# Performance work log

Measured on AMD Instinct MI355X. Metric: run time of the kernel, lower is better.

## Reference

```python
import jax, jax.numpy as jnp
import numpy as np

N, DEG, F_IN, H = 50000, 16, 128, 32
E = N * DEG


def _linear_params(key, out_f, in_f):
    kw, kb = jax.random.split(key)
    s = 1.0 / np.sqrt(in_f)
    W = jax.random.uniform(kw, (out_f, in_f), jnp.float32, -s, s)
    b = jax.random.uniform(kb, (out_f,), jnp.float32, -s, s)
    return W, b


def setup_inputs() -> dict:
    key = jax.random.key(0)
    ks = jax.random.split(key, 12)
    X = jax.random.normal(ks[0], (N, F_IN), jnp.float32)
    # DEG distinct nonzero offsets shared by all rows -> unique (src,dst) pairs,
    # so the COO tensor is already coalesced (no duplicate indices).
    offsets = jax.random.permutation(ks[1], jnp.arange(1, N))[:DEG]
    src = jnp.repeat(jnp.arange(N, dtype=jnp.int32), DEG)
    dst = ((src.reshape(N, DEG) + offsets[None, :].astype(jnp.int32)) % N).reshape(-1)
    D = jax.ops.segment_sum(jnp.ones((E,), jnp.float32), src, num_segments=N)
    wn1p, bn1p = _linear_params(ks[2], H, F_IN)      # convN1.pass_map
    wn1s, bn1s = _linear_params(ks[3], H, F_IN)      # convN1.self_map
    we1p, be1p = _linear_params(ks[4], H, 2 * H)     # convE1.pass_map
    we1s, be1s = _linear_params(ks[5], H, F_IN)      # convE1.self_map
    wn2p, bn2p = _linear_params(ks[6], H, H)         # convN2.pass_map
    wn2s, bn2s = _linear_params(ks[7], H, H)         # convN2.self_map
    we2p, be2p = _linear_params(ks[8], H, 2 * H)     # convE2.pass_map
    we2s, be2s = _linear_params(ks[9], H, H)         # convE2.self_map
    wc, bc = _linear_params(ks[10], 1, H)            # classifier
    return dict(X=X, src=src, dst=dst, D=D,
                wn1p=wn1p, bn1p=bn1p, wn1s=wn1s, bn1s=bn1s,
                we1p=we1p, be1p=be1p, we1s=we1s, be1s=be1s,
                wn2p=wn2p, bn2p=bn2p, wn2s=wn2s, bn2s=bn2s,
                we2p=we2p, be2p=be2p, we2s=we2s, be2s=be2s,
                wc=wc, bc=bc)


def reference(X, src, dst, D,
              wn1p, bn1p, wn1s, bn1s,
              we1p, be1p, we1s, be1s,
              wn2p, bn2p, wn2s, bn2s,
              we2p, be2p, we2s, be2s,
              wc, bc):
    n = X.shape[0]

    def node_conv(vals, Xn, wp, bp, ws, bs):
        # torch.sparse.sum(A, dim=1): sum edge values per source row
        Asum = jax.ops.segment_sum(vals, src, num_segments=n)
        return jax.nn.relu((Asum / D[:, None]) @ wp.T + bp + Xn @ ws.T + bs)

    def edge_conv(vals, Xn, wp, bp, ws, bs):
        X1, X2 = Xn[src], Xn[dst]
        Ef = jnp.concatenate([(X1 - X2) * 0.5, (X1 + X2) * 0.5], axis=-1)
        return jax.nn.relu(Ef @ wp.T + bp + vals @ ws.T + bs)

    # add_graph: edge features = |X[src] - X[dst]|
    vals0 = jnp.abs(X[src] - X[dst])            # (E, F_IN)
    X0 = jnp.zeros_like(X)                       # forward zeros node features
    Xn1 = node_conv(vals0, X0, wn1p, bn1p, wn1s, bn1s)   # (N, 32)
    vals1 = edge_conv(vals0, Xn1, we1p, be1p, we1s, be1s)  # (E, 32)
    Xn2 = node_conv(vals1, Xn1, wn2p, bn2p, wn2s, bn2s)  # (N, 32)
    vals2 = edge_conv(vals1, Xn2, we2p, be2p, we2s, be2s)  # (E, 32)
    SX = jax.nn.sigmoid(vals2 @ wc.T + bc)[:, 0]          # (E,)
    return SX
```

## Files before the change

### kernel.cpp

```cpp
#include <hip/hip_runtime.h>

#define DEG 16
#define F_IN 128
#define H 32

typedef __attribute__((ext_vector_type(8))) _Float16 f16x8;
typedef __attribute__((ext_vector_type(4))) float f32x4;
typedef __attribute__((ext_vector_type(4))) int i32x4;

union HS  { _Float16 f; unsigned short s; };
union HF4 { _Float16 h[4]; uint2 u; };

__device__ __forceinline__ float relu_f(float x) { return fmaxf(x, 0.0f); }

__device__ __forceinline__ f16x8 habs8(f16x8 a) {
    union { f16x8 h; i32x4 i; } u; u.h = a;
#pragma unroll
    for (int k = 0; k < 4; ++k) u.i[k] &= 0x7FFF7FFF;
    return u.h;
}

__global__ __launch_bounds__(256) void k_xhalf(
    const float* __restrict__ X, _Float16* __restrict__ Xh, long n8)
{
    const long t = (long)blockIdx.x * 256 + threadIdx.x;
    if (t >= n8) return;
    const float4* p = (const float4*)X + t * 2;
    const float4 a = p[0], b = p[1];
    f16x8 h;
    h[0] = (_Float16)a.x; h[1] = (_Float16)a.y; h[2] = (_Float16)a.z; h[3] = (_Float16)a.w;
    h[4] = (_Float16)b.x; h[5] = (_Float16)b.y; h[6] = (_Float16)b.z; h[7] = (_Float16)b.w;
    *(f16x8*)(Xh + t * 8) = h;
}

__global__ __launch_bounds__(256) void k_prep(
    const float* __restrict__ we1s, const float* __restrict__ we1p,
    const float* __restrict__ be1p, const float* __restrict__ be1s,
    const float* __restrict__ we2p, const float* __restrict__ we2s,
    const float* __restrict__ be2p, const float* __restrict__ be2s,
    const float* __restrict__ wn1p, const float* __restrict__ bn1p,
    const float* __restrict__ bn1s,
    const float* __restrict__ wn2p, const float* __restrict__ bn2p,
    const float* __restrict__ wn2s, const float* __restrict__ bn2s,
    _Float16* __restrict__ Wcat1, _Float16* __restrict__ Wcat2,
    _Float16* __restrict__ Wn1ph,
    _Float16* __restrict__ Wn2ph, _Float16* __restrict__ Wn2sh,
    float* __restrict__ bias1, float* __restrict__ bias2,
    float* __restrict__ biasn1, float* __restrict__ biasn2)
{
    const int t0 = blockIdx.x * 256 + threadIdx.x;
    const int stride = gridDim.x * 256;
    for (int idx = t0; idx < 32 * 192; idx += stride) {
        const int n = idx / 192, k = idx - n * 192;
        float w;
        if (k < 128)       w = we1s[n * 128 + k];
        else if (k < 160)  w = 0.5f * we1p[n * 64 + (k - 128)];
        else               w = 0.5f * we1p[n * 64 + 32 + (k - 160)];
        Wcat1[idx] = (_Float16)w;
    }
    for (int idx = t0; idx < 32 * 96; idx += stride) {
        const int n = idx / 96, k = idx - n * 96;
        float w;
        if (k < 32)       w = 0.5f * we2p[n * 64 + k];
        else if (k < 64)  w = 0.5f * we2p[n * 64 + 32 + (k - 32)];
        else              w = we2s[n * 32 + (k - 64)];
        Wcat2[idx] = (_Float16)w;
    }
    for (int idx = t0; idx < 32 * 128; idx += stride)
        Wn1ph[idx] = (_Float16)wn1p[idx];
    for (int idx = t0; idx < 32 * 32; idx += stride) {
        Wn2ph[idx] = (_Float16)wn2p[idx];
        Wn2sh[idx] = (_Float16)wn2s[idx];
    }
    if (t0 < H) {
        bias1[t0]  = be1p[t0] + be1s[t0];
        bias2[t0]  = be2p[t0] + be2s[t0];
        biasn1[t0] = bn1p[t0] + bn1s[t0];
        biasn2[t0] = bn2p[t0] + bn2s[t0];
    }
}

__global__ __launch_bounds__(64, 3) void k_p1(
    const _Float16* __restrict__ Xh, const int* __restrict__ dst,
    const float* __restrict__ D,
    const _Float16* __restrict__ Wcat1, const _Float16* __restrict__ Wn1ph,
    const float* __restrict__ biasn1,
    _Float16* __restrict__ t1h, _Float16* __restrict__ Xn1h, int N)
{
    const int lane = threadIdx.x;
    const int m = lane & 15, g = lane >> 4;
    const int i0 = blockIdx.x * 16;
    const int srow = (i0 + m < N) ? (i0 + m) : (N - 1);

    i32x4 dj4[4];
    {
        const i32x4* dp = (const i32x4*)(dst + (size_t)srow * DEG);
#pragma unroll
        for (int q = 0; q < 4; ++q) dj4[q] = dp[q];
    }
    f16x8 sv[4];
#pragma unroll
    for (int kb = 0; kb < 4; ++kb)
        sv[kb] = *(const f16x8*)(Xh + (size_t)srow * F_IN + kb * 32 + g * 8);
    f16x8 Bs[4][2], Bn[4][2];
#pragma unroll
    for (int kb = 0; kb < 4; ++kb)
#pragma unroll
        for (int t = 0; t < 2; ++t) {
            Bs[kb][t] = *(const f16x8*)(Wcat1 + (t * 16 + m) * 192 + kb * 32 + g * 8);
            Bn[kb][t] = *(const f16x8*)(Wn1ph + (t * 16 + m) * 128 + kb * 32 + g * 8);
        }

    f16x8 tvc[4], tvn[4];
#pragma unroll
    for (int kb = 0; kb < 4; ++kb)
        tvc[kb] = *(const f16x8*)(Xh + (size_t)dj4[0][0] * F_IN + kb * 32 + g * 8);

    f32x4 cn0 = {0.f,0.f,0.f,0.f}, cn1 = {0.f,0.f,0.f,0.f};
#pragma unroll
    for (int j = 0; j < 16; ++j) {
        if (j < 15) {
            const int dn = dj4[(j + 1) >> 2][(j + 1) & 3];
#pragma unroll
            for (int kb = 0; kb < 4; ++kb)
                tvn[kb] = *(const f16x8*)(Xh + (size_t)dn * F_IN + kb * 32 + g * 8);
        }
        f32x4 cs0 = {0.f,0.f,0.f,0.f}, cs1 = {0.f,0.f,0.f,0.f};
#pragma unroll
        for (int kb = 0; kb < 4; ++kb) {
            const f16x8 a = habs8(sv[kb] - tvc[kb]);
            cs0 = __builtin_amdgcn_mfma_f32_16x16x32_f16(a, Bs[kb][0], cs0, 0, 0, 0);
            cs1 = __builtin_amdgcn_mfma_f32_16x16x32_f16(a, Bs[kb][1], cs1, 0, 0, 0);
            cn0 = __builtin_amdgcn_mfma_f32_16x16x32_f16(a, Bn[kb][0], cn0, 0, 0, 0);
            cn1 = __builtin_amdgcn_mfma_f32_16x16x32_f16(a, Bn[kb][1], cn1, 0, 0, 0);
        }
        const size_t tb = ((size_t)blockIdx.x * 16 + j) * 512;
        HF4 a;
#pragma unroll
        for (int r = 0; r < 4; ++r) a.h[r] = (_Float16)cs0[r];
        *(uint2*)(t1h + tb + lane * 4) = a.u;
#pragma unroll
        for (int r = 0; r < 4; ++r) a.h[r] = (_Float16)cs1[r];
        *(uint2*)(t1h + tb + 256 + lane * 4) = a.u;
#pragma unroll
        for (int kb = 0; kb < 4; ++kb) tvc[kb] = tvn[kb];
    }
    const float bn0 = biasn1[m], bn1v = biasn1[16 + m];
#pragma unroll
    for (int r = 0; r < 4; ++r) {
        const int node = i0 + g * 4 + r;
        if (node < N) {
            const float invD = 1.0f / D[node];
            Xn1h[(size_t)node * H + m]      = (_Float16)relu_f(cn0[r] * invD + bn0);
            Xn1h[(size_t)node * H + 16 + m] = (_Float16)relu_f(cn1[r] * invD + bn1v);
        }
    }
}

__global__ __launch_bounds__(64, 4) void k_p2(
    const int* __restrict__ dst, const _Float16* __restrict__ Xn1h,
    const _Float16* __restrict__ Wcat1, const float* __restrict__ bias1,
    const _Float16* __restrict__ Wn2ph, const _Float16* __restrict__ Wn2sh,
    const float* __restrict__ biasn2, const float* __restrict__ D,
    _Float16* t1v1,
    _Float16* __restrict__ Xn2h, int N)
{
    __shared__ unsigned short RP[16 * 40];
    const int lane = threadIdx.x;
    const int m = lane & 15, g = lane >> 4;
    const int i0 = blockIdx.x * 16;
    const int srow = (i0 + m < N) ? (i0 + m) : (N - 1);

    i32x4 dj4[4];
    {
        const i32x4* dp = (const i32x4*)(dst + (size_t)srow * DEG);
#pragma unroll
        for (int q = 0; q < 4; ++q) dj4[q] = dp[q];
    }
    const f16x8 x1 = *(const f16x8*)(Xn1h + (size_t)srow * H + g * 8);
    f16x8 Bf[2][2];
#pragma unroll
    for (int kb = 0; kb < 2; ++kb)
#pragma unroll
        for (int t = 0; t < 2; ++t)
            Bf[kb][t] = *(const f16x8*)(Wcat1 + (t * 16 + m) * 192 + (4 + kb) * 32 + g * 8);

    f16x8 x2c, x2n;
    uint2 u0c, u1c, u0n, u1n;
    {
        const int d0 = dj4[0][0];
        x2c = *(const f16x8*)(Xn1h + (size_t)d0 * H + g * 8);
        const size_t tb = ((size_t)blockIdx.x * 16) * 512;
        u0c = *(const uint2*)(t1v1 + tb + lane * 4);
        u1c = *(const uint2*)(t1v1 + tb + 256 + lane * 4);
    }
    const float b0 = bias1[m], b1v = bias1[16 + m];
    f32x4 sB0 = {0.f,0.f,0.f,0.f}, sB1 = {0.f,0.f,0.f,0.f};
    const int rr = lane >> 2, qq = lane & 3;
#pragma unroll
    for (int j = 0; j < 16; ++j) {
        if (j < 15) {
            const int dn = dj4[(j + 1) >> 2][(j + 1) & 3];
            x2n = *(const f16x8*)(Xn1h + (size_t)dn * H + g * 8);
            const size_t tbn = ((size_t)blockIdx.x * 16 + j + 1) * 512;
            u0n = *(const uint2*)(t1v1 + tbn + lane * 4);
            u1n = *(const uint2*)(t1v1 + tbn + 256 + lane * 4);
        }
        f32x4 c0, c1;
        { HF4 a; a.u = u0c;
#pragma unroll
          for (int r = 0; r < 4; ++r) c0[r] = (float)a.h[r];
          a.u = u1c;
#pragma unroll
          for (int r = 0; r < 4; ++r) c1[r] = (float)a.h[r]; }
        const f16x8 ad = x1 - x2c;
        const f16x8 aS = x1 + x2c;
        c0 = __builtin_amdgcn_mfma_f32_16x16x32_f16(ad, Bf[0][0], c0, 0, 0, 0);
        c1 = __builtin_amdgcn_mfma_f32_16x16x32_f16(ad, Bf[0][1], c1, 0, 0, 0);
        c0 = __builtin_amdgcn_mfma_f32_16x16x32_f16(aS, Bf[1][0], c0, 0, 0, 0);
        c1 = __builtin_amdgcn_mfma_f32_16x16x32_f16(aS, Bf[1][1], c1, 0, 0, 0);
#pragma unroll
        for (int r = 0; r < 4; ++r) {
            const float v0 = relu_f(c0[r] + b0);
            const float v1 = relu_f(c1[r] + b1v);
            HS h0, h1; h0.f = (_Float16)v0; h1.f = (_Float16)v1;
            RP[(g * 4 + r) * 40 + m]      = h0.s;
            RP[(g * 4 + r) * 40 + 16 + m] = h1.s;
            sB0[r] += v0; sB1[r] += v1;
        }
        const size_t tb = ((size_t)blockIdx.x * 16 + j) * 512;
        const i32x4 v = *(const i32x4*)(RP + rr * 40 + qq * 8);
        *(i32x4*)(t1v1 + tb + rr * 32 + qq * 8) = v;
        x2c = x2n; u0c = u0n; u1c = u1n;
    }
    _Float16* RPh = (_Float16*)RP;
#pragma unroll
    for (int r = 0; r < 4; ++r) {
        const int node = i0 + g * 4 + r;
        const float invD = 1.0f / D[(node < N) ? node : (N - 1)];
        RPh[(g * 4 + r) * 40 + m]      = (_Float16)(sB0[r] * invD);
        RPh[(g * 4 + r) * 40 + 16 + m] = (_Float16)(sB1[r] * invD);
    }
    const f16x8 aF = *(const f16x8*)(RPh + m * 40 + g * 8);
    f16x8 Bp[2], Bs2[2];
#pragma unroll
    for (int t = 0; t < 2; ++t) {
        Bp[t]  = *(const f16x8*)(Wn2ph + (t * 16 + m) * H + g * 8);
        Bs2[t] = *(const f16x8*)(Wn2sh + (t * 16 + m) * H + g * 8);
    }
    f32x4 c0 = {0.f,0.f,0.f,0.f}, c1 = {0.f,0.f,0.f,0.f};
    c0 = __builtin_amdgcn_mfma_f32_16x16x32_f16(aF, Bp[0], c0, 0, 0, 0);
    c1 = __builtin_amdgcn_mfma_f32_16x16x32_f16(aF, Bp[1], c1, 0, 0, 0);
    c0 = __builtin_amdgcn_mfma_f32_16x16x32_f16(x1, Bs2[0], c0, 0, 0, 0);
    c1 = __builtin_amdgcn_mfma_f32_16x16x32_f16(x1, Bs2[1], c1, 0, 0, 0);
    const float bp0 = biasn2[m], bp1 = biasn2[16 + m];
#pragma unroll
    for (int r = 0; r < 4; ++r) {
        const int node = i0 + g * 4 + r;
        if (node < N) {
            Xn2h[(size_t)node * H + m]      = (_Float16)relu_f(c0[r] + bp0);
            Xn2h[(size_t)node * H + 16 + m] = (_Float16)relu_f(c1[r] + bp1);
        }
    }
}

__global__ __launch_bounds__(64, 4) void k_p3(
    const _Float16* __restrict__ Xn2h, const int* __restrict__ dst,
    const _Float16* __restrict__ vals1,
    const _Float16* __restrict__ Wcat2, const float* __restrict__ bias2,
    const float* __restrict__ wc, const float* __restrict__ bc,
    float* __restrict__ out, int N)
{
    __shared__ float outS[16 * 16];
    const int lane = threadIdx.x;
    const int m = lane & 15, g = lane >> 4;
    const int i0 = blockIdx.x * 16;
    const int srow = (i0 + m < N) ? (i0 + m) : (N - 1);

    i32x4 dj4[4];
    {
        const i32x4* dp = (const i32x4*)(dst + (size_t)srow * DEG);
#pragma unroll
        for (int q = 0; q < 4; ++q) dj4[q] = dp[q];
    }
    const f16x8 x1 = *(const f16x8*)(Xn2h + (size_t)srow * H + g * 8);
    f16x8 Bf[3][2];
#pragma unroll
    for (int kb = 0; kb < 3; ++kb)
#pragma unroll
        for (int t = 0; t < 2; ++t)
            Bf[kb][t] = *(const f16x8*)(Wcat2 + (t * 16 + m) * 96 + kb * 32 + g * 8);

    f16x8 x2b[2], avb[2];
#pragma unroll
    for (int s = 0; s < 2; ++s) {
        const int dn = dj4[s >> 2][s & 3];
        x2b[s] = *(const f16x8*)(Xn2h + (size_t)dn * H + g * 8);
        avb[s] = *(const f16x8*)(vals1 + ((size_t)blockIdx.x * 16 + s) * 512 + m * 32 + g * 8);
    }
    const float b0 = bias2[m], b1v = bias2[16 + m];
    const float w0 = wc[m], w1 = wc[16 + m];
#pragma unroll
    for (int j = 0; j < 16; ++j) {
        const int s = j & 1;
        const f16x8 x2 = x2b[s];
        const f16x8 av = avb[s];
        if (j < 14) {
            const int dn = dj4[(j + 2) >> 2][(j + 2) & 3];
            x2b[s] = *(const f16x8*)(Xn2h + (size_t)dn * H + g * 8);
            avb[s] = *(const f16x8*)(vals1 + ((size_t)blockIdx.x * 16 + j + 2) * 512 + m * 32 + g * 8);
        }
        const f16x8 ad = x1 - x2;
        const f16x8 aS = x1 + x2;
        f32x4 c0 = {0.f,0.f,0.f,0.f}, c1 = {0.f,0.f,0.f,0.f};
        c0 = __builtin_amdgcn_mfma_f32_16x16x32_f16(ad, Bf[0][0], c0, 0, 0, 0);
        c1 = __builtin_amdgcn_mfma_f32_16x16x32_f16(ad, Bf[0][1], c1, 0, 0, 0);
        c0 = __builtin_amdgcn_mfma_f32_16x16x32_f16(aS, Bf[1][0], c0, 0, 0, 0);
        c1 = __builtin_amdgcn_mfma_f32_16x16x32_f16(aS, Bf[1][1], c1, 0, 0, 0);
        c0 = __builtin_amdgcn_mfma_f32_16x16x32_f16(av, Bf[2][0], c0, 0, 0, 0);
        c1 = __builtin_amdgcn_mfma_f32_16x16x32_f16(av, Bf[2][1], c1, 0, 0, 0);

        float sr[4];
#pragma unroll
        for (int r = 0; r < 4; ++r)
            sr[r] = relu_f(c0[r] + b0) * w0 + relu_f(c1[r] + b1v) * w1;
#pragma unroll
        for (int mask = 1; mask < 16; mask <<= 1) {
#pragma unroll
            for (int r = 0; r < 4; ++r)
                sr[r] += __shfl_xor(sr[r], mask);
        }
        if (m == 0) {
#pragma unroll
            for (int r = 0; r < 4; ++r)
                outS[(g * 4 + r) * 16 + j] = sr[r];
        }
    }
    {
        const float bcv = bc[0];
        const float* s = outS + lane * 4;
        float4 o;
        o.x = 1.0f / (1.0f + __expf(-(s[0] + bcv)));
        o.y = 1.0f / (1.0f + __expf(-(s[1] + bcv)));
        o.z = 1.0f / (1.0f + __expf(-(s[2] + bcv)));
        o.w = 1.0f / (1.0f + __expf(-(s[3] + bcv)));
        if (i0 + 16 <= N || (i0 + (lane >> 2)) < N)
            *(float4*)(out + (size_t)i0 * DEG + lane * 4) = o;
    }
}

extern "C" void kernel_launch(void* const* d_in, const int* in_sizes, int n_in,
                              void* d_out, int out_size, void* d_ws, size_t ws_size,
                              hipStream_t stream)
{
    const float* X    = (const float*)d_in[0];
    const int*   dst  = (const int*)  d_in[2];
    const float* D    = (const float*)d_in[3];
    const float* wn1p = (const float*)d_in[4];
    const float* bn1p = (const float*)d_in[5];
    const float* bn1s = (const float*)d_in[7];
    const float* we1p = (const float*)d_in[8];
    const float* be1p = (const float*)d_in[9];
    const float* we1s = (const float*)d_in[10];
    const float* be1s = (const float*)d_in[11];
    const float* wn2p = (const float*)d_in[12];
    const float* bn2p = (const float*)d_in[13];
    const float* wn2s = (const float*)d_in[14];
    const float* bn2s = (const float*)d_in[15];
    const float* we2p = (const float*)d_in[16];
    const float* be2p = (const float*)d_in[17];
    const float* we2s = (const float*)d_in[18];
    const float* be2s = (const float*)d_in[19];
    const float* wc   = (const float*)d_in[20];
    const float* bc   = (const float*)d_in[21];

    const int N = in_sizes[3];
    const int nbW = (N + 15) / 16;
    const size_t Epad = (size_t)nbW * 16 * DEG;

    char* w = (char*)d_ws;
    _Float16* t1v1  = (_Float16*)w;  w += Epad * H * 2;
    _Float16* Xh    = (_Float16*)w;  w += (size_t)N * F_IN * 2;
    _Float16* Xn1h  = (_Float16*)w;  w += (size_t)N * H * 2;
    _Float16* Xn2h  = (_Float16*)w;  w += (size_t)N * H * 2;
    _Float16* Wcat1 = (_Float16*)w;  w += 32 * 192 * 2;
    _Float16* Wcat2 = (_Float16*)w;  w += 32 * 96 * 2;
    _Float16* Wn1ph = (_Float16*)w;  w += 32 * 128 * 2;
    _Float16* Wn2ph = (_Float16*)w;  w += 32 * 32 * 2;
    _Float16* Wn2sh = (_Float16*)w;  w += 32 * 32 * 2;
    float* bias1  = (float*)w;       w += H * 4;
    float* bias2  = (float*)w;       w += H * 4;
    float* biasn1 = (float*)w;       w += H * 4;
    float* biasn2 = (float*)w;       w += H * 4;
    float* outp = (float*)d_out;

    const long n8 = (long)N * F_IN / 8;
    const int nbX = (int)((n8 + 255) / 256);

    k_xhalf<<<nbX, 256, 0, stream>>>(X, Xh, n8);
    k_prep<<<32, 256, 0, stream>>>(we1s, we1p, be1p, be1s, we2p, we2s, be2p, be2s,
                                   wn1p, bn1p, bn1s, wn2p, bn2p, wn2s, bn2s,
                                   Wcat1, Wcat2, Wn1ph, Wn2ph, Wn2sh,
                                   bias1, bias2, biasn1, biasn2);
    k_p1<<<nbW, 64, 0, stream>>>(Xh, dst, D, Wcat1, Wn1ph, biasn1, t1v1, Xn1h, N);
    k_p2<<<nbW, 64, 0, stream>>>(dst, Xn1h, Wcat1, bias1, Wn2ph, Wn2sh,
                                 biasn2, D, t1v1, Xn2h, N);
    k_p3<<<nbW, 64, 0, stream>>>(Xn2h, dst, t1v1, Wcat2, bias2, wc, bc, outp, N);
}
```

Before: 197.9 us.

## Split each 16-row tile's edge loop across four waves and merge prep kernels

```diff
diff --git a/kernel.cpp b/kernel.cpp
--- a/kernel.cpp
+++ b/kernel.cpp
@@ -20,20 +20,8 @@
     return u.h;
 }
 
-__global__ __launch_bounds__(256) void k_xhalf(
-    const float* __restrict__ X, _Float16* __restrict__ Xh, long n8)
-{
-    const long t = (long)blockIdx.x * 256 + threadIdx.x;
-    if (t >= n8) return;
-    const float4* p = (const float4*)X + t * 2;
-    const float4 a = p[0], b = p[1];
-    f16x8 h;
-    h[0] = (_Float16)a.x; h[1] = (_Float16)a.y; h[2] = (_Float16)a.z; h[3] = (_Float16)a.w;
-    h[4] = (_Float16)b.x; h[5] = (_Float16)b.y; h[6] = (_Float16)b.z; h[7] = (_Float16)b.w;
-    *(f16x8*)(Xh + t * 8) = h;
-}
-
-__global__ __launch_bounds__(256) void k_prep(
+__global__ __launch_bounds__(256) void k_pre(
+    const float* __restrict__ X, _Float16* __restrict__ Xh, long n8,
     const float* __restrict__ we1s, const float* __restrict__ we1p,
     const float* __restrict__ be1p, const float* __restrict__ be1s,
     const float* __restrict__ we2p, const float* __restrict__ we2s,
@@ -48,8 +36,19 @@
     float* __restrict__ bias1, float* __restrict__ bias2,
     float* __restrict__ biasn1, float* __restrict__ biasn2)
 {
+    if (blockIdx.x >= 32) {
+        const long t = (long)(blockIdx.x - 32) * 256 + threadIdx.x;
+        if (t >= n8) return;
+        const float4* p = (const float4*)X + t * 2;
+        const float4 a = p[0], b = p[1];
+        f16x8 h;
+        h[0] = (_Float16)a.x; h[1] = (_Float16)a.y; h[2] = (_Float16)a.z; h[3] = (_Float16)a.w;
+        h[4] = (_Float16)b.x; h[5] = (_Float16)b.y; h[6] = (_Float16)b.z; h[7] = (_Float16)b.w;
+        *(f16x8*)(Xh + t * 8) = h;
+        return;
+    }
     const int t0 = blockIdx.x * 256 + threadIdx.x;
-    const int stride = gridDim.x * 256;
+    const int stride = 32 * 256;
     for (int idx = t0; idx < 32 * 192; idx += stride) {
         const int n = idx / 192, k = idx - n * 192;
         float w;
@@ -80,24 +79,23 @@
     }
 }
 
-__global__ __launch_bounds__(64, 3) void k_p1(
+__global__ __launch_bounds__(256, 3) void k_p1(
     const _Float16* __restrict__ Xh, const int* __restrict__ dst,
     const float* __restrict__ D,
     const _Float16* __restrict__ Wcat1, const _Float16* __restrict__ Wn1ph,
     const float* __restrict__ biasn1,
     _Float16* __restrict__ t1h, _Float16* __restrict__ Xn1h, int N)
 {
-    const int lane = threadIdx.x;
+    __shared__ float red[4][8][64];
+    const int tid = threadIdx.x;
+    const int lane = tid & 63;
+    const int w = tid >> 6;
     const int m = lane & 15, g = lane >> 4;
     const int i0 = blockIdx.x * 16;
     const int srow = (i0 + m < N) ? (i0 + m) : (N - 1);
 
-    i32x4 dj4[4];
-    {
-        const i32x4* dp = (const i32x4*)(dst + (size_t)srow * DEG);
-#pragma unroll
-        for (int q = 0; q < 4; ++q) dj4[q] = dp[q];
-    }
+    const i32x4 dj = ((const i32x4*)(dst + (size_t)srow * DEG))[w];
+
     f16x8 sv[4];
 #pragma unroll
     for (int kb = 0; kb < 4; ++kb)
@@ -114,13 +112,13 @@
     f16x8 tvc[4], tvn[4];
 #pragma unroll
     for (int kb = 0; kb < 4; ++kb)
-        tvc[kb] = *(const f16x8*)(Xh + (size_t)dj4[0][0] * F_IN + kb * 32 + g * 8);
+        tvc[kb] = *(const f16x8*)(Xh + (size_t)dj[0] * F_IN + kb * 32 + g * 8);
 
     f32x4 cn0 = {0.f,0.f,0.f,0.f}, cn1 = {0.f,0.f,0.f,0.f};
 #pragma unroll
-    for (int j = 0; j < 16; ++j) {
-        if (j < 15) {
-            const int dn = dj4[(j + 1) >> 2][(j + 1) & 3];
+    for (int jj = 0; jj < 4; ++jj) {
+        if (jj < 3) {
+            const int dn = dj[jj + 1];
 #pragma unroll
             for (int kb = 0; kb < 4; ++kb)
                 tvn[kb] = *(const f16x8*)(Xh + (size_t)dn * F_IN + kb * 32 + g * 8);
@@ -134,30 +132,42 @@
             cn0 = __builtin_amdgcn_mfma_f32_16x16x32_f16(a, Bn[kb][0], cn0, 0, 0, 0);
             cn1 = __builtin_amdgcn_mfma_f32_16x16x32_f16(a, Bn[kb][1], cn1, 0, 0, 0);
         }
-        const size_t tb = ((size_t)blockIdx.x * 16 + j) * 512;
-        HF4 a;
-#pragma unroll
-        for (int r = 0; r < 4; ++r) a.h[r] = (_Float16)cs0[r];
-        *(uint2*)(t1h + tb + lane * 4) = a.u;
-#pragma unroll
-        for (int r = 0; r < 4; ++r) a.h[r] = (_Float16)cs1[r];
-        *(uint2*)(t1h + tb + 256 + lane * 4) = a.u;
+        const size_t tb = ((size_t)blockIdx.x * 16 + w * 4 + jj) * 512;
+        HF4 a4;
+#pragma unroll
+        for (int r = 0; r < 4; ++r) a4.h[r] = (_Float16)cs0[r];
+        *(uint2*)(t1h + tb + lane * 4) = a4.u;
+#pragma unroll
+        for (int r = 0; r < 4; ++r) a4.h[r] = (_Float16)cs1[r];
+        *(uint2*)(t1h + tb + 256 + lane * 4) = a4.u;
 #pragma unroll
         for (int kb = 0; kb < 4; ++kb) tvc[kb] = tvn[kb];
     }
-    const float bn0 = biasn1[m], bn1v = biasn1[16 + m];
 #pragma unroll
     for (int r = 0; r < 4; ++r) {
-        const int node = i0 + g * 4 + r;
-        if (node < N) {
-            const float invD = 1.0f / D[node];
-            Xn1h[(size_t)node * H + m]      = (_Float16)relu_f(cn0[r] * invD + bn0);
-            Xn1h[(size_t)node * H + 16 + m] = (_Float16)relu_f(cn1[r] * invD + bn1v);
-        }
-    }
-}
-
-__global__ __launch_bounds__(64, 4) void k_p2(
+        red[w][r][lane]     = cn0[r];
+        red[w][4 + r][lane] = cn1[r];
+    }
+    __syncthreads();
+    if (w == 0) {
+        const float bn0 = biasn1[m], bn1v = biasn1[16 + m];
+#pragma unroll
+        for (int r = 0; r < 4; ++r) {
+            const int node = i0 + g * 4 + r;
+            if (node < N) {
+                const float invD = 1.0f / D[node];
+                const float a0 = red[0][r][lane] + red[1][r][lane]
+                               + red[2][r][lane] + red[3][r][lane];
+                const float a1 = red[0][4+r][lane] + red[1][4+r][lane]
+                               + red[2][4+r][lane] + red[3][4+r][lane];
+                Xn1h[(size_t)node * H + m]      = (_Float16)relu_f(a0 * invD + bn0);
+                Xn1h[(size_t)node * H + 16 + m] = (_Float16)relu_f(a1 * invD + bn1v);
+            }
+        }
+    }
+}
+
+__global__ __launch_bounds__(256, 4) void k_p2(
     const int* __restrict__ dst, const _Float16* __restrict__ Xn1h,
     const _Float16* __restrict__ Wcat1, const float* __restrict__ bias1,
     const _Float16* __restrict__ Wn2ph, const _Float16* __restrict__ Wn2sh,
@@ -165,18 +175,16 @@
     _Float16* t1v1,
     _Float16* __restrict__ Xn2h, int N)
 {
-    __shared__ unsigned short RP[16 * 40];
-    const int lane = threadIdx.x;
+    __shared__ unsigned short RP[4][16 * 40];
+    __shared__ float red[4][8][64];
+    const int tid = threadIdx.x;
+    const int lane = tid & 63;
+    const int w = tid >> 6;
     const int m = lane & 15, g = lane >> 4;
     const int i0 = blockIdx.x * 16;
     const int srow = (i0 + m < N) ? (i0 + m) : (N - 1);
 
-    i32x4 dj4[4];
-    {
-        const i32x4* dp = (const i32x4*)(dst + (size_t)srow * DEG);
-#pragma unroll
-        for (int q = 0; q < 4; ++q) dj4[q] = dp[q];
-    }
+    const i32x4 dj = ((const i32x4*)(dst + (size_t)srow * DEG))[w];
     const f16x8 x1 = *(const f16x8*)(Xn1h + (size_t)srow * H + g * 8);
     f16x8 Bf[2][2];
 #pragma unroll
@@ -188,21 +196,22 @@
     f16x8 x2c, x2n;
     uint2 u0c, u1c, u0n, u1n;
     {
-        const int d0 = dj4[0][0];
+        const int d0 = dj[0];
         x2c = *(const f16x8*)(Xn1h + (size_t)d0 * H + g * 8);
-        const size_t tb = ((size_t)blockIdx.x * 16) * 512;
+        const size_t tb = ((size_t)blockIdx.x * 16 + w * 4) * 512;
         u0c = *(const uint2*)(t1v1 + tb + lane * 4);
         u1c = *(const uint2*)(t1v1 + tb + 256 + lane * 4);
     }
     const float b0 = bias1[m], b1v = bias1[16 + m];
     f32x4 sB0 = {0.f,0.f,0.f,0.f}, sB1 = {0.f,0.f,0.f,0.f};
     const int rr = lane >> 2, qq = lane & 3;
-#pragma unroll
-    for (int j = 0; j < 16; ++j) {
-        if (j < 15) {
-            const int dn = dj4[(j + 1) >> 2][(j + 1) & 3];
+    unsigned short* RPw = RP[w];
+#pragma unroll
+    for (int jj = 0; jj < 4; ++jj) {
+        if (jj < 3) {
+            const int dn = dj[jj + 1];
             x2n = *(const f16x8*)(Xn1h + (size_t)dn * H + g * 8);
-            const size_t tbn = ((size_t)blockIdx.x * 16 + j + 1) * 512;
+            const size_t tbn = ((size_t)blockIdx.x * 16 + w * 4 + jj + 1) * 512;
             u0n = *(const uint2*)(t1v1 + tbn + lane * 4);
             u1n = *(const uint2*)(t1v1 + tbn + 256 + lane * 4);
         }
@@ -224,47 +233,59 @@
             const float v0 = relu_f(c0[r] + b0);
             const float v1 = relu_f(c1[r] + b1v);
             HS h0, h1; h0.f = (_Float16)v0; h1.f = (_Float16)v1;
-            RP[(g * 4 + r) * 40 + m]      = h0.s;
-            RP[(g * 4 + r) * 40 + 16 + m] = h1.s;
+            RPw[(g * 4 + r) * 40 + m]      = h0.s;
+            RPw[(g * 4 + r) * 40 + 16 + m] = h1.s;
             sB0[r] += v0; sB1[r] += v1;
         }
-        const size_t tb = ((size_t)blockIdx.x * 16 + j) * 512;
-        const i32x4 v = *(const i32x4*)(RP + rr * 40 + qq * 8);
+        const size_t tb = ((size_t)blockIdx.x * 16 + w * 4 + jj) * 512;
+        const i32x4 v = *(const i32x4*)(RPw + rr * 40 + qq * 8);
         *(i32x4*)(t1v1 + tb + rr * 32 + qq * 8) = v;
         x2c = x2n; u0c = u0n; u1c = u1n;
     }
-    _Float16* RPh = (_Float16*)RP;
 #pragma unroll
     for (int r = 0; r < 4; ++r) {
-        const int node = i0 + g * 4 + r;
-        const float invD = 1.0f / D[(node < N) ? node : (N - 1)];
-        RPh[(g * 4 + r) * 40 + m]      = (_Float16)(sB0[r] * invD);
-        RPh[(g * 4 + r) * 40 + 16 + m] = (_Float16)(sB1[r] * invD);
-    }
-    const f16x8 aF = *(const f16x8*)(RPh + m * 40 + g * 8);
-    f16x8 Bp[2], Bs2[2];
-#pragma unroll
-    for (int t = 0; t < 2; ++t) {
-        Bp[t]  = *(const f16x8*)(Wn2ph + (t * 16 + m) * H + g * 8);
-        Bs2[t] = *(const f16x8*)(Wn2sh + (t * 16 + m) * H + g * 8);
-    }
-    f32x4 c0 = {0.f,0.f,0.f,0.f}, c1 = {0.f,0.f,0.f,0.f};
-    c0 = __builtin_amdgcn_mfma_f32_16x16x32_f16(aF, Bp[0], c0, 0, 0, 0);
-    c1 = __builtin_amdgcn_mfma_f32_16x16x32_f16(aF, Bp[1], c1, 0, 0, 0);
-    c0 = __builtin_amdgcn_mfma_f32_16x16x32_f16(x1, Bs2[0], c0, 0, 0, 0);
-    c1 = __builtin_amdgcn_mfma_f32_16x16x32_f16(x1, Bs2[1], c1, 0, 0, 0);
-    const float bp0 = biasn2[m], bp1 = biasn2[16 + m];
-#pragma unroll
-    for (int r = 0; r < 4; ++r) {
-        const int node = i0 + g * 4 + r;
-        if (node < N) {
-            Xn2h[(size_t)node * H + m]      = (_Float16)relu_f(c0[r] + bp0);
-            Xn2h[(size_t)node * H + 16 + m] = (_Float16)relu_f(c1[r] + bp1);
-        }
-    }
-}
-
-__global__ __launch_bounds__(64, 4) void k_p3(
+        red[w][r][lane]     = sB0[r];
+        red[w][4 + r][lane] = sB1[r];
+    }
+    __syncthreads();
+    if (w == 0) {
+        _Float16* RPh = (_Float16*)RP[0];
+#pragma unroll
+        for (int r = 0; r < 4; ++r) {
+            const int node = i0 + g * 4 + r;
+            const float invD = 1.0f / D[(node < N) ? node : (N - 1)];
+            const float a0 = red[0][r][lane] + red[1][r][lane]
+                           + red[2][r][lane] + red[3][r][lane];
+            const float a1 = red[0][4+r][lane] + red[1][4+r][lane]
+                           + red[2][4+r][lane] + red[3][4+r][lane];
+            RPh[(g * 4 + r) * 40 + m]      = (_Float16)(a0 * invD);
+            RPh[(g * 4 + r) * 40 + 16 + m] = (_Float16)(a1 * invD);
+        }
+        const f16x8 aF = *(const f16x8*)(RPh + m * 40 + g * 8);
+        f16x8 Bp[2], Bs2[2];
+#pragma unroll
+        for (int t = 0; t < 2; ++t) {
+            Bp[t]  = *(const f16x8*)(Wn2ph + (t * 16 + m) * H + g * 8);
+            Bs2[t] = *(const f16x8*)(Wn2sh + (t * 16 + m) * H + g * 8);
+        }
+        f32x4 c0 = {0.f,0.f,0.f,0.f}, c1 = {0.f,0.f,0.f,0.f};
+        c0 = __builtin_amdgcn_mfma_f32_16x16x32_f16(aF, Bp[0], c0, 0, 0, 0);
+        c1 = __builtin_amdgcn_mfma_f32_16x16x32_f16(aF, Bp[1], c1, 0, 0, 0);
+        c0 = __builtin_amdgcn_mfma_f32_16x16x32_f16(x1, Bs2[0], c0, 0, 0, 0);
+        c1 = __builtin_amdgcn_mfma_f32_16x16x32_f16(x1, Bs2[1], c1, 0, 0, 0);
+        const float bp0 = biasn2[m], bp1 = biasn2[16 + m];
+#pragma unroll
+        for (int r = 0; r < 4; ++r) {
+            const int node = i0 + g * 4 + r;
+            if (node < N) {
+                Xn2h[(size_t)node * H + m]      = (_Float16)relu_f(c0[r] + bp0);
+                Xn2h[(size_t)node * H + 16 + m] = (_Float16)relu_f(c1[r] + bp1);
+            }
+        }
+    }
+}
+
+__global__ __launch_bounds__(256, 4) void k_p3(
     const _Float16* __restrict__ Xn2h, const int* __restrict__ dst,
     const _Float16* __restrict__ vals1,
     const _Float16* __restrict__ Wcat2, const float* __restrict__ bias2,
@@ -272,17 +293,14 @@
     float* __restrict__ out, int N)
 {
     __shared__ float outS[16 * 16];
-    const int lane = threadIdx.x;
+    const int tid = threadIdx.x;
+    const int lane = tid & 63;
+    const int w = tid >> 6;
     const int m = lane & 15, g = lane >> 4;
     const int i0 = blockIdx.x * 16;
     const int srow = (i0 + m < N) ? (i0 + m) : (N - 1);
 
-    i32x4 dj4[4];
-    {
-        const i32x4* dp = (const i32x4*)(dst + (size_t)srow * DEG);
-#pragma unroll
-        for (int q = 0; q < 4; ++q) dj4[q] = dp[q];
-    }
+    const i32x4 dj = ((const i32x4*)(dst + (size_t)srow * DEG))[w];
     const f16x8 x1 = *(const f16x8*)(Xn2h + (size_t)srow * H + g * 8);
     f16x8 Bf[3][2];
 #pragma unroll
@@ -294,21 +312,21 @@
     f16x8 x2b[2], avb[2];
 #pragma unroll
     for (int s = 0; s < 2; ++s) {
-        const int dn = dj4[s >> 2][s & 3];
+        const int dn = dj[s];
         x2b[s] = *(const f16x8*)(Xn2h + (size_t)dn * H + g * 8);
-        avb[s] = *(const f16x8*)(vals1 + ((size_t)blockIdx.x * 16 + s) * 512 + m * 32 + g * 8);
+        avb[s] = *(const f16x8*)(vals1 + ((size_t)blockIdx.x * 16 + w * 4 + s) * 512 + m * 32 + g * 8);
     }
     const float b0 = bias2[m], b1v = bias2[16 + m];
     const float w0 = wc[m], w1 = wc[16 + m];
 #pragma unroll
-    for (int j = 0; j < 16; ++j) {
-        const int s = j & 1;
+    for (int jj = 0; jj < 4; ++jj) {
+        const int s = jj & 1;
         const f16x8 x2 = x2b[s];
         const f16x8 av = avb[s];
-        if (j < 14) {
-            const int dn = dj4[(j + 2) >> 2][(j + 2) & 3];
+        if (jj < 2) {
+            const int dn = dj[jj + 2];
             x2b[s] = *(const f16x8*)(Xn2h + (size_t)dn * H + g * 8);
-            avb[s] = *(const f16x8*)(vals1 + ((size_t)blockIdx.x * 16 + j + 2) * 512 + m * 32 + g * 8);
+            avb[s] = *(const f16x8*)(vals1 + ((size_t)blockIdx.x * 16 + w * 4 + jj + 2) * 512 + m * 32 + g * 8);
         }
         const f16x8 ad = x1 - x2;
         const f16x8 aS = x1 + x2;
@@ -333,19 +351,16 @@
         if (m == 0) {
 #pragma unroll
             for (int r = 0; r < 4; ++r)
-                outS[(g * 4 + r) * 16 + j] = sr[r];
-        }
-    }
+                outS[(g * 4 + r) * 16 + (w * 4 + jj)] = sr[r];
+        }
+    }
+    __syncthreads();
     {
         const float bcv = bc[0];
-        const float* s = outS + lane * 4;
-        float4 o;
-        o.x = 1.0f / (1.0f + __expf(-(s[0] + bcv)));
-        o.y = 1.0f / (1.0f + __expf(-(s[1] + bcv)));
-        o.z = 1.0f / (1.0f + __expf(-(s[2] + bcv)));
-        o.w = 1.0f / (1.0f + __expf(-(s[3] + bcv)));
-        if (i0 + 16 <= N || (i0 + (lane >> 2)) < N)
-            *(float4*)(out + (size_t)i0 * DEG + lane * 4) = o;
+        const float v = outS[tid];
+        const float o = 1.0f / (1.0f + __expf(-(v + bcv)));
+        if (i0 + 16 <= N || (i0 + (tid >> 4)) < N)
+            out[(size_t)i0 * DEG + tid] = o;
     }
 }
 
@@ -397,13 +412,13 @@
     const long n8 = (long)N * F_IN / 8;
     const int nbX = (int)((n8 + 255) / 256);
 
-    k_xhalf<<<nbX, 256, 0, stream>>>(X, Xh, n8);
-    k_prep<<<32, 256, 0, stream>>>(we1s, we1p, be1p, be1s, we2p, we2s, be2p, be2s,
-                                   wn1p, bn1p, bn1s, wn2p, bn2p, wn2s, bn2s,
-                                   Wcat1, Wcat2, Wn1ph, Wn2ph, Wn2sh,
-                                   bias1, bias2, biasn1, biasn2);
-    k_p1<<<nbW, 64, 0, stream>>>(Xh, dst, D, Wcat1, Wn1ph, biasn1, t1v1, Xn1h, N);
-    k_p2<<<nbW, 64, 0, stream>>>(dst, Xn1h, Wcat1, bias1, Wn2ph, Wn2sh,
-                                 biasn2, D, t1v1, Xn2h, N);
-    k_p3<<<nbW, 64, 0, stream>>>(Xn2h, dst, t1v1, Wcat2, bias2, wc, bc, outp, N);
-}
+    k_pre<<<nbX + 32, 256, 0, stream>>>(X, Xh, n8,
+                                        we1s, we1p, be1p, be1s, we2p, we2s, be2p, be2s,
+                                        wn1p, bn1p, bn1s, wn2p, bn2p, wn2s, bn2s,
+                                        Wcat1, Wcat2, Wn1ph, Wn2ph, Wn2sh,
+                                        bias1, bias2, biasn1, biasn2);
+    k_p1<<<nbW, 256, 0, stream>>>(Xh, dst, D, Wcat1, Wn1ph, biasn1, t1v1, Xn1h, N);
+    k_p2<<<nbW, 256, 0, stream>>>(dst, Xn1h, Wcat1, bias1, Wn2ph, Wn2sh,
+                                  biasn2, D, t1v1, Xn2h, N);
+    k_p3<<<nbW, 256, 0, stream>>>(Xn2h, dst, t1v1, Wcat2, bias2, wc, bc, outp, N);
+}
```

New measurement: 210.3 us. 6.2% more time.
